# Performance work log

Hardware: AMD Instinct MI355X
Metric: run time of the kernel (lower is better)

Reference implementation:

```python
import jax, jax.numpy as jnp
import numpy as np

B, C, H, W = 4, 256, 128, 128
K = 3
BN = max(16, C // 4)  # 64
PAD = K // 2
EPS = 1e-5


def conv2d(x, w, b=None, pad=0):
    out = jax.lax.conv_general_dilated(
        x, w, (1, 1), [(pad, pad), (pad, pad)],
        dimension_numbers=("NCHW", "OIHW", "NCHW"))
    if b is not None:
        out = out + b[None, :, None, None]
    return out


def deform_conv2d(z, offset, mask, w, b):
    # torchvision modulated deform conv v2: offset [B,2*K*K,H,W] interleaved (dy,dx),
    # mask [B,K*K,H,W], kernel positions row-major, stride 1, pad PAD.
    Bz, Cb, Hz, Wz = z.shape
    K2 = K * K
    off = offset.reshape(Bz, K2, 2, Hz, Wz)
    ky, kx = jnp.meshgrid(jnp.arange(K), jnp.arange(K), indexing="ij")
    # sampling positions py/px: [B, K2, H, W]
    py = off[:, :, 0] + jnp.arange(Hz)[None, None, :, None] + (ky.reshape(K2) - PAD)[None, :, None, None]
    px = off[:, :, 1] + jnp.arange(Wz)[None, None, None, :] + (kx.reshape(K2) - PAD)[None, :, None, None]
    y0 = jnp.floor(py)
    x0 = jnp.floor(px)
    wy1 = py - y0  # frac weights
    wx1 = px - x0
    z_flat = z.reshape(Bz, Cb, Hz * Wz)

    def gather(yy, xx, wgt):
        valid = (yy >= 0) & (yy < Hz) & (xx >= 0) & (xx < Wz)
        yc = jnp.clip(yy, 0, Hz - 1).astype(jnp.int32)
        xc = jnp.clip(xx, 0, Wz - 1).astype(jnp.int32)
        idx = (yc * Wz + xc).reshape(Bz, K2 * Hz * Wz)
        g = jnp.take_along_axis(z_flat, idx[:, None, :], axis=2)  # [B, Cb, K2*H*W]
        g = g.reshape(Bz, Cb, K2, Hz, Wz)
        return g * (wgt * valid.astype(z.dtype))[:, None]

    val = (gather(y0, x0, (1 - wy1) * (1 - wx1))
           + gather(y0, x0 + 1, (1 - wy1) * wx1)
           + gather(y0 + 1, x0, wy1 * (1 - wx1))
           + gather(y0 + 1, x0 + 1, wy1 * wx1))
    val = val * mask[:, None]  # modulate: [B, Cb, K2, H, W]
    out = jnp.einsum("bckhw,ock->bohw", val, w.reshape(w.shape[0], Cb, K2))
    return out + b[None, :, None, None]


def setup_inputs() -> dict:
    key = jax.random.key(0)
    ks = jax.random.split(key, 11)
    s = 0.05
    return {
        "x": jax.random.normal(ks[0], (B, C, H, W), jnp.float32),
        "down_w": jax.random.normal(ks[1], (BN, C, 1, 1), jnp.float32) * s,
        "off_w": jax.random.normal(ks[2], (2 * K * K, BN, 3, 3), jnp.float32) * s,
        "off_b": jax.random.normal(ks[3], (2 * K * K,), jnp.float32) * s,
        "mask_w": jax.random.normal(ks[4], (K * K, BN, 3, 3), jnp.float32) * s,
        "mask_b": jax.random.normal(ks[5], (K * K,), jnp.float32) * s,
        "def_w": jax.random.normal(ks[6], (BN, BN, K, K), jnp.float32) * s,
        "def_b": jax.random.normal(ks[7], (BN,), jnp.float32) * s,
        "up_w": jax.random.normal(ks[8], (C, BN, 1, 1), jnp.float32) * s,
        "gamma": jnp.ones((C,), jnp.float32),
        "beta": jnp.zeros((C,), jnp.float32),
    }


def reference(x, down_w, off_w, off_b, mask_w, mask_b, def_w, def_b, up_w, gamma, beta):
    z = conv2d(x, down_w)                               # 1x1 down: [B, BN, H, W]
    offset = conv2d(z, off_w, off_b, pad=1)             # [B, 18, H, W]
    mask = jax.nn.sigmoid(conv2d(z, mask_w, mask_b, pad=1))  # [B, 9, H, W]
    z = deform_conv2d(z, offset, mask, def_w, def_b)    # [B, BN, H, W]
    z = conv2d(z, up_w)                                 # 1x1 up: [B, C, H, W]
    y = x + z
    # BatchNorm2d in training mode: batch statistics over (B, H, W), biased var
    mean = jnp.mean(y, axis=(0, 2, 3), keepdims=True)
    var = jnp.var(y, axis=(0, 2, 3), keepdims=True)
    yh = (y - mean) * jax.lax.rsqrt(var + EPS)
    yh = yh * gamma[None, :, None, None] + beta[None, :, None, None]
    return yh * jax.nn.sigmoid(yh)  # SiLU
```

## Files before the change

kernel.cpp:

```cpp
#include <hip/hip_runtime.h>
#include <hip/hip_bf16.h>


typedef __attribute__((ext_vector_type(8))) short bf16x8;
typedef __attribute__((ext_vector_type(4))) short bf16x4;
typedef __attribute__((ext_vector_type(4))) float f32x4;

#define HW   16384
#define CC   256
#define BNC  64

#define WS_STATS   0
#define WS_SS      131072
#define WS_FD      135168
#define WS_FOM     167936
#define WS_FDEF    204800
#define WS_FUP     278528
#define WS_ZBF     311296
#define WS_OM      8699904
#define WS_Z2      15777792

__device__ __forceinline__ short f2b(float f) {
    unsigned u = __float_as_uint(f);
    unsigned r = (u + 0x7FFFu + ((u >> 16) & 1u)) >> 16;
    return (short)r;
}
__device__ __forceinline__ float b2f(short s) {
    return __uint_as_float(((unsigned)(unsigned short)s) << 16);
}

__global__ void k_prep(const float* __restrict__ down_w, const float* __restrict__ off_w,
                       const float* __restrict__ mask_w, const float* __restrict__ def_w,
                       const float* __restrict__ up_w, char* __restrict__ ws) {
    int g = blockIdx.x * 256 + threadIdx.x;
    int row = g >> 6, lane = g & 63;
    if (row >= 172) return;
    int l15 = lane & 15, q = lane >> 4;
    short vals[8];
    short* dst;
    if (row < 32) {
        int nt = row >> 3, kk = row & 7;
        int n = nt * 16 + l15;
        for (int j = 0; j < 8; ++j) {
            int c = kk * 32 + q * 8 + j;
            vals[j] = f2b(down_w[n * 256 + c]);
        }
        dst = (short*)(ws + WS_FD) + row * 512 + lane * 8;
    } else if (row < 68) {
        int r = row - 32; int nt = r / 18, kk = r % 18;
        int n = nt * 16 + l15;
        for (int j = 0; j < 8; ++j) {
            int kap = kk * 32 + q * 8 + j; int k = kap >> 6, c = kap & 63;
            float v = 0.f;
            if (n < 18)      v = off_w[(n * 64 + c) * 9 + k];
            else if (n < 27) v = mask_w[((n - 18) * 64 + c) * 9 + k];
            vals[j] = f2b(v);
        }
        dst = (short*)(ws + WS_FOM) + r * 512 + lane * 8;
    } else if (row < 140) {
        int r = row - 68; int nt = r / 18, kk = r % 18;
        int n = nt * 16 + l15;
        int u = kk * 4 + q, k = u >> 3;
        for (int j = 0; j < 8; ++j) {
            int c = (u & 7) * 8 + j;
            vals[j] = f2b(def_w[(n * 64 + c) * 9 + k]);
        }
        dst = (short*)(ws + WS_FDEF) + r * 512 + lane * 8;
    } else {
        int r = row - 140; int nt = r >> 1, kk = r & 1;
        int o = nt * 16 + l15;
        for (int j = 0; j < 8; ++j) {
            int c = kk * 32 + q * 8 + j;
            vals[j] = f2b(up_w[o * 64 + c]);
        }
        dst = (short*)(ws + WS_FUP) + r * 512 + lane * 8;
    }
    for (int j = 0; j < 8; ++j) dst[j] = vals[j];
}

__global__ __launch_bounds__(256) void k_down(const float* __restrict__ x,
                                              const short* __restrict__ wfd,
                                              short* __restrict__ zbf) {
    __shared__ __align__(16) short xl[64 * 264];
    int blk = blockIdx.x;
    int b = blk >> 8;
    int hw0 = (blk & 255) * 64;
    int t = threadIdx.x;
    const float* xb = x + (size_t)b * CC * HW + hw0;
    int px = t & 63, w = t >> 6;
    for (int h = 0; h < 8; ++h) {
        int c0 = h * 32 + w * 8;
        bf16x8 pk;
        #pragma unroll
        for (int j = 0; j < 8; ++j)
            pk[j] = f2b(xb[(size_t)(c0 + j) * HW + px]);
        *(bf16x8*)(&xl[px * 264 + c0]) = pk;
    }
    __syncthreads();
    int lane = t & 63, wv = t >> 6;
    int l15 = lane & 15, q = lane >> 4;
    bf16x8 A[8];
    const short* xrow = &xl[(wv * 16 + l15) * 264];
    for (int kk = 0; kk < 8; ++kk)
        A[kk] = *(const bf16x8*)(xrow + kk * 32 + q * 8);
    const bf16x8* Bp = (const bf16x8*)wfd;
    size_t obase = ((size_t)b * HW + hw0 + wv * 16) * 64;
    for (int nt = 0; nt < 4; ++nt) {
        f32x4 acc = {0.f, 0.f, 0.f, 0.f};
        for (int kk = 0; kk < 8; ++kk) {
            bf16x8 Bf = Bp[(nt * 8 + kk) * 64 + lane];
            acc = __builtin_amdgcn_mfma_f32_16x16x32_bf16(A[kk], Bf, acc, 0, 0, 0);
        }
        int n = nt * 16 + l15;
        for (int r = 0; r < 4; ++r) {
            int prow = q * 4 + r;
            zbf[obase + (size_t)prow * 64 + n] = f2b(acc[r]);
        }
    }
}

__global__ __launch_bounds__(256) void k_offmask(const short* __restrict__ zbf,
                                                 const short* __restrict__ wfom,
                                                 const float* __restrict__ off_b,
                                                 const float* __restrict__ mask_b,
                                                 float* __restrict__ om) {
    int blk = blockIdx.x;
    int b = blk >> 8;
    int hw0 = (blk & 255) * 64;
    int y = hw0 >> 7, x0 = hw0 & 127;
    int t = threadIdx.x, lane = t & 63, wv = t >> 6;
    int l15 = lane & 15, q = lane >> 4;
    int xx0 = x0 + wv * 16 + l15;
    const short* zb = zbf + (size_t)b * HW * 64;
    f32x4 acc0 = {0, 0, 0, 0}, acc1 = {0, 0, 0, 0};
    const bf16x8* Bp = (const bf16x8*)wfom;
    for (int kk = 0; kk < 18; ++kk) {
        int k = kk >> 1;
        int yy = y + (k / 3) - 1;
        int xx = xx0 + (k % 3) - 1;
        int c0 = (kk & 1) * 32 + q * 8;
        bf16x8 A = {0, 0, 0, 0, 0, 0, 0, 0};
        if (yy >= 0 && yy < 128 && xx >= 0 && xx < 128)
            A = *(const bf16x8*)(zb + ((size_t)(yy * 128 + xx)) * 64 + c0);
        bf16x8 B0 = Bp[kk * 64 + lane];
        bf16x8 B1 = Bp[(18 + kk) * 64 + lane];
        acc0 = __builtin_amdgcn_mfma_f32_16x16x32_bf16(A, B0, acc0, 0, 0, 0);
        acc1 = __builtin_amdgcn_mfma_f32_16x16x32_bf16(A, B1, acc1, 0, 0, 0);
    }
    float* omb = om + ((size_t)b * HW + hw0 + wv * 16) * 27;
    for (int half = 0; half < 2; ++half) {
        f32x4 acc = half ? acc1 : acc0;
        int n = half * 16 + l15;
        if (n < 27) {
            for (int r = 0; r < 4; ++r) {
                int prow = q * 4 + r;
                float v = acc[r];
                if (n < 18) v += off_b[n];
                else { v += mask_b[n - 18]; v = 1.f / (1.f + __expf(-v)); }
                omb[prow * 27 + n] = v;
            }
        }
    }
}

__global__ __launch_bounds__(256) void k_deform(const short* __restrict__ zbf,
                                                const float* __restrict__ om,
                                                const short* __restrict__ wfdef,
                                                const float* __restrict__ def_b,
                                                short* __restrict__ z2) {
    __shared__ __align__(16) short ldsZ[169 * 64];
    __shared__ int4   pAi4[144];
    __shared__ float4 pAw4[144];
    __shared__ int    pAf[144];
    __shared__ __align__(16) short valA[18 * 64 * 8];
    int blk = blockIdx.x;
    int b = blk >> 10;
    int tile = blk & 1023;
    int yt = (tile >> 5) << 2, xt = (tile & 31) << 2;
    int sy0 = yt - 4; sy0 = sy0 < 0 ? 0 : (sy0 > 115 ? 115 : sy0);
    int sx0 = xt - 4; sx0 = sx0 < 0 ? 0 : (sx0 > 115 ? 115 : sx0);
    int t = threadIdx.x;
    const short* zbs = zbf + (size_t)b * HW * 64;
    for (int u = t; u < 1352; u += 256) {
        int r = u / 104, rem = u - r * 104;
        int p = rem >> 3, cg = rem & 7;
        int gp = (sy0 + r) * 128 + sx0 + p;
        int lpix = r * 13 + p;
        int slot = (cg + lpix) & 7;
        *(int4*)(&ldsZ[lpix * 64 + slot * 8]) = *(const int4*)(zbs + (size_t)gp * 64 + cg * 8);
    }
    if (t < 144) {
        int px = t / 9, k = t % 9;
        int oy = yt + (px >> 2), ox = xt + (px & 3);
        const float* p = om + ((size_t)b * HW + oy * 128 + ox) * 27;
        float dy = p[2 * k], dx = p[2 * k + 1], m = p[18 + k];
        float py  = (float)oy + (float)(k / 3 - 1) + dy;
        float pxf = (float)ox + (float)(k % 3 - 1) + dx;
        float fy = floorf(py), fx = floorf(pxf);
        int iy = (int)fy, ix = (int)fx;
        float wy = py - fy, wx = pxf - fx;
        float ww[4] = { (1.f - wy) * (1.f - wx) * m, (1.f - wy) * wx * m,
                        wy * (1.f - wx) * m,          wy * wx * m };
        bool flg = (iy >= sy0) && (iy + 1 <= sy0 + 12) && (ix >= sx0) && (ix + 1 <= sx0 + 12);
        int ys[2] = {iy, iy + 1}, xs[2] = {ix, ix + 1};
        int   ri[4]; float rw[4];
        for (int ci = 0; ci < 4; ++ci) {
            int cy = ys[ci >> 1], cx = xs[ci & 1];
            if (flg) {
                int lp = (cy - sy0) * 13 + (cx - sx0);
                ri[ci] = (lp << 6) | (lp & 7);
                rw[ci] = ww[ci];
            } else {
                bool v = (cy >= 0 && cy < 128 && cx >= 0 && cx < 128);
                ri[ci] = v ? (cy * 128 + cx) * 64 : 0;
                rw[ci] = v ? ww[ci] : 0.f;
            }
        }
        pAi4[t] = make_int4(ri[0], ri[1], ri[2], ri[3]);
        pAw4[t] = make_float4(rw[0], rw[1], rw[2], rw[3]);
        pAf[t]  = flg ? 1 : 0;
    }
    __syncthreads();
    for (int it = 0; it < 5; ++it) {
        int s = t + it * 256;
        if (s < 1152) {
            int px = s & 15, u = s >> 4;
            int k = u >> 3, cg = u & 7;
            int task = px * 9 + k;
            int4   idx = pAi4[task];
            float4 wt  = pAw4[task];
            int    flg = pAf[task];
            int   ii[4] = { idx.x, idx.y, idx.z, idx.w };
            float wwt[4] = { wt.x, wt.y, wt.z, wt.w };
            int cgs = cg * 8;
            float acc[8] = {0.f, 0.f, 0.f, 0.f, 0.f, 0.f, 0.f, 0.f};
            #pragma unroll
            for (int ci = 0; ci < 4; ++ci) {
                float w = wwt[ci];
                int4 d;
                if (flg) {
                    int v = ii[ci];
                    d = *(const int4*)(&ldsZ[(v & ~63) + (((cg + (v & 7)) & 7) << 3)]);
                } else {
                    d = *(const int4*)(zbs + ii[ci] + cgs);
                }
                int dp[4] = { d.x, d.y, d.z, d.w };
                #pragma unroll
                for (int p = 0; p < 4; ++p) {
                    float lo = __uint_as_float((unsigned)dp[p] << 16);
                    float hi = __uint_as_float((unsigned)dp[p] & 0xffff0000u);
                    acc[2 * p]     += w * lo;
                    acc[2 * p + 1] += w * hi;
                }
            }
            bf16x8 out;
            #pragma unroll
            for (int j = 0; j < 8; ++j) out[j] = f2b(acc[j]);
            *(bf16x8*)(&valA[s * 8]) = out;
        }
    }
    __syncthreads();
    int lane = t & 63, wv = t >> 6;
    int l15 = lane & 15, q = lane >> 4;
    f32x4 acc = {0, 0, 0, 0};
    const bf16x8* Bp = (const bf16x8*)wfdef;
    const bf16x8* Ap = (const bf16x8*)valA;
    for (int kk = 0; kk < 18; ++kk) {
        bf16x8 A  = Ap[kk * 64 + lane];
        bf16x8 Bf = Bp[(wv * 18 + kk) * 64 + lane];
        acc = __builtin_amdgcn_mfma_f32_16x16x32_bf16(A, Bf, acc, 0, 0, 0);
    }
    int n = wv * 16 + l15;
    float bias = def_b[n];
    short* z2b = z2 + (size_t)b * HW * 64;
    for (int r = 0; r < 4; ++r) {
        int prow = q * 4 + r;
        int hw = (yt + (prow >> 2)) * 128 + xt + (prow & 3);
        z2b[(size_t)hw * 64 + n] = f2b(acc[r] + bias);
    }
}

__global__ __launch_bounds__(256) void k_up(const short* __restrict__ z2,
                                            const short* __restrict__ wfup,
                                            const float* __restrict__ x,
                                            float* __restrict__ yout,
                                            float* __restrict__ stats) {
    __shared__ __align__(16) short yl[256 * 70];
    int blk = blockIdx.x;
    int b = blk >> 8;
    int hw0 = (blk & 255) * 64;
    int t = threadIdx.x, lane = t & 63, wv = t >> 6;
    int l15 = lane & 15, q = lane >> 4;
    const short* z2b = z2 + ((size_t)b * HW + hw0 + wv * 16) * 64;
    bf16x8 A0 = *(const bf16x8*)(z2b + (size_t)l15 * 64 + q * 8);
    bf16x8 A1 = *(const bf16x8*)(z2b + (size_t)l15 * 64 + 32 + q * 8);
    const bf16x8* Bp = (const bf16x8*)wfup;
    for (int nt = 0; nt < 16; ++nt) {
        f32x4 acc = {0, 0, 0, 0};
        acc = __builtin_amdgcn_mfma_f32_16x16x32_bf16(A0, Bp[(nt * 2 + 0) * 64 + lane], acc, 0, 0, 0);
        acc = __builtin_amdgcn_mfma_f32_16x16x32_bf16(A1, Bp[(nt * 2 + 1) * 64 + lane], acc, 0, 0, 0);
        int o = nt * 16 + l15;
        bf16x4 pk;
        #pragma unroll
        for (int r = 0; r < 4; ++r) pk[r] = f2b(acc[r]);
        *(bf16x4*)(&yl[o * 70 + wv * 16 + q * 4]) = pk;
    }
    __syncthreads();
    int i16 = t & 15, og = t >> 4;
    int bucket = blk & 63;
    size_t base = (size_t)b * CC * HW + hw0 + (size_t)i16 * 4;
    #pragma unroll
    for (int i = 0; i < 16; ++i) {
        int o = og + 16 * i;
        size_t pb = base + (size_t)o * HW;
        float4 xv = *(const float4*)(x + pb);
        bf16x4 uv = *(const bf16x4*)(&yl[o * 70 + i16 * 4]);
        float v0 = b2f(uv[0]) + xv.x;
        float v1 = b2f(uv[1]) + xv.y;
        float v2 = b2f(uv[2]) + xv.z;
        float v3 = b2f(uv[3]) + xv.w;
        *(float4*)(yout + pb) = make_float4(v0, v1, v2, v3);
        float s  = v0 + v1 + v2 + v3;
        float s2 = v0 * v0 + v1 * v1 + v2 * v2 + v3 * v3;
        #pragma unroll
        for (int m = 8; m >= 1; m >>= 1) { s += __shfl_xor(s, m); s2 += __shfl_xor(s2, m); }
        if (i16 == 0) {
            atomicAdd(&stats[bucket * 512 + o], s);
            atomicAdd(&stats[bucket * 512 + 256 + o], s2);
        }
    }
}

__global__ void k_stats(const float* __restrict__ stats, const float* __restrict__ gamma,
                        const float* __restrict__ beta, float* __restrict__ ss) {
    int o = threadIdx.x;
    float s = 0.f, s2 = 0.f;
    for (int u = 0; u < 64; ++u) { s += stats[u * 512 + o]; s2 += stats[u * 512 + 256 + o]; }
    float mean = s * (1.f / 65536.f);
    float var  = s2 * (1.f / 65536.f) - mean * mean;
    float rs = rsqrtf(var + 1e-5f);
    float sc = gamma[o] * rs;
    ss[o]       = sc;
    ss[256 + o] = beta[o] - mean * sc;
}

__global__ __launch_bounds__(256) void k_bn(float* __restrict__ y, const float* __restrict__ ss) {
    int g = blockIdx.x * 256 + threadIdx.x;
    int o = (g >> 10) & 255;
    float sc = ss[o], sh = ss[256 + o];
    float4* p = (float4*)y + (size_t)g * 4;
    for (int i = 0; i < 4; ++i) {
        float4 v = p[i];
        float vf[4] = { v.x, v.y, v.z, v.w };
        for (int j = 0; j < 4; ++j) {
            float h = vf[j] * sc + sh;
            vf[j] = h / (1.f + __expf(-h));
        }
        p[i] = make_float4(vf[0], vf[1], vf[2], vf[3]);
    }
}

extern "C" void kernel_launch(void* const* d_in, const int* in_sizes, int n_in,
                              void* d_out, int out_size, void* d_ws, size_t ws_size,
                              hipStream_t stream) {
    const float* x      = (const float*)d_in[0];
    const float* down_w = (const float*)d_in[1];
    const float* off_w  = (const float*)d_in[2];
    const float* off_b  = (const float*)d_in[3];
    const float* mask_w = (const float*)d_in[4];
    const float* mask_b = (const float*)d_in[5];
    const float* def_w  = (const float*)d_in[6];
    const float* def_b  = (const float*)d_in[7];
    const float* up_w   = (const float*)d_in[8];
    const float* gamma  = (const float*)d_in[9];
    const float* beta   = (const float*)d_in[10];
    char* ws = (char*)d_ws;
    float* stats = (float*)(ws + WS_STATS);
    float* ss    = (float*)(ws + WS_SS);
    short* wfd   = (short*)(ws + WS_FD);
    short* wfom  = (short*)(ws + WS_FOM);
    short* wfdef = (short*)(ws + WS_FDEF);
    short* wfup  = (short*)(ws + WS_FUP);
    short* zbf   = (short*)(ws + WS_ZBF);
    float* om    = (float*)(ws + WS_OM);
    short* z2    = (short*)(ws + WS_Z2);
    float* y     = (float*)d_out;

    hipMemsetAsync(stats, 0, 64 * 512 * sizeof(float), stream);
    hipLaunchKernelGGL(k_prep,    dim3(43),   dim3(256), 0, stream, down_w, off_w, mask_w, def_w, up_w, ws);
    hipLaunchKernelGGL(k_down,    dim3(1024), dim3(256), 0, stream, x, wfd, zbf);
    hipLaunchKernelGGL(k_offmask, dim3(1024), dim3(256), 0, stream, zbf, wfom, off_b, mask_b, om);
    hipLaunchKernelGGL(k_deform,  dim3(4096), dim3(256), 0, stream, zbf, om, wfdef, def_b, z2);
    hipLaunchKernelGGL(k_up,      dim3(1024), dim3(256), 0, stream, z2, wfup, x, y, stats);
    hipLaunchKernelGGL(k_stats,   dim3(1),    dim3(256), 0, stream, stats, gamma, beta, ss);
    hipLaunchKernelGGL(k_bn,      dim3(4096), dim3(256), 0, stream, y, ss);
}
```

Measured before the change: 246.5 us.

## Fuse BN stats and SiLU apply into up-projection kernel via grid barrier

The up-projection kernel now keeps its residual-sum outputs in registers, then uses an atomic-counter grid-wide barrier: the last block computes the BatchNorm scale/shift and every block spins until it is published, then applies BN and SiLU and writes the output once. This removes the separate stats and BN kernels along with the write-then-reread round trip of the 64 MB output tensor. In exchange it relies on all 1024 blocks being co-resident (launch bounds of 4 blocks per CU), which is required to avoid deadlock, and it raises register pressure by holding 16 float4 values per thread.

```diff
diff --git a/kernel.cpp b/kernel.cpp
--- a/kernel.cpp
+++ b/kernel.cpp
@@ -11,7 +11,8 @@
 #define BNC  64
 
 #define WS_STATS   0
-#define WS_SS      131072
+#define WS_CNT     131072
+#define WS_SSG     131136
 #define WS_FD      135168
 #define WS_FOM     167936
 #define WS_FDEF    204800
@@ -280,12 +281,18 @@
     }
 }
 
-__global__ __launch_bounds__(256) void k_up(const short* __restrict__ z2,
-                                            const short* __restrict__ wfup,
-                                            const float* __restrict__ x,
-                                            float* __restrict__ yout,
-                                            float* __restrict__ stats) {
+__global__ __launch_bounds__(256, 4) void k_up(const short* __restrict__ z2,
+                                               const short* __restrict__ wfup,
+                                               const float* __restrict__ x,
+                                               const float* __restrict__ gamma,
+                                               const float* __restrict__ beta,
+                                               float* __restrict__ yout,
+                                               float* __restrict__ stats,
+                                               unsigned* __restrict__ cnt,
+                                               float* __restrict__ ssG) {
     __shared__ __align__(16) short yl[256 * 70];
+    __shared__ float ssl[512];
+    __shared__ int lflag;
     int blk = blockIdx.x;
     int b = blk >> 8;
     int hw0 = (blk & 255) * 64;
@@ -309,6 +316,7 @@
     int i16 = t & 15, og = t >> 4;
     int bucket = blk & 63;
     size_t base = (size_t)b * CC * HW + hw0 + (size_t)i16 * 4;
+    float4 v[16];
     #pragma unroll
     for (int i = 0; i < 16; ++i) {
         int o = og + 16 * i;
@@ -319,7 +327,7 @@
         float v1 = b2f(uv[1]) + xv.y;
         float v2 = b2f(uv[2]) + xv.z;
         float v3 = b2f(uv[3]) + xv.w;
-        *(float4*)(yout + pb) = make_float4(v0, v1, v2, v3);
+        v[i] = make_float4(v0, v1, v2, v3);
         float s  = v0 + v1 + v2 + v3;
         float s2 = v0 * v0 + v1 * v1 + v2 * v2 + v3 * v3;
         #pragma unroll
@@ -329,34 +337,50 @@
             atomicAdd(&stats[bucket * 512 + 256 + o], s2);
         }
     }
-}
-
-__global__ void k_stats(const float* __restrict__ stats, const float* __restrict__ gamma,
-                        const float* __restrict__ beta, float* __restrict__ ss) {
-    int o = threadIdx.x;
-    float s = 0.f, s2 = 0.f;
-    for (int u = 0; u < 64; ++u) { s += stats[u * 512 + o]; s2 += stats[u * 512 + 256 + o]; }
-    float mean = s * (1.f / 65536.f);
-    float var  = s2 * (1.f / 65536.f) - mean * mean;
-    float rs = rsqrtf(var + 1e-5f);
-    float sc = gamma[o] * rs;
-    ss[o]       = sc;
-    ss[256 + o] = beta[o] - mean * sc;
-}
-
-__global__ __launch_bounds__(256) void k_bn(float* __restrict__ y, const float* __restrict__ ss) {
-    int g = blockIdx.x * 256 + threadIdx.x;
-    int o = (g >> 10) & 255;
-    float sc = ss[o], sh = ss[256 + o];
-    float4* p = (float4*)y + (size_t)g * 4;
-    for (int i = 0; i < 4; ++i) {
-        float4 v = p[i];
-        float vf[4] = { v.x, v.y, v.z, v.w };
-        for (int j = 0; j < 4; ++j) {
-            float h = vf[j] * sc + sh;
-            vf[j] = h / (1.f + __expf(-h));
-        }
-        p[i] = make_float4(vf[0], vf[1], vf[2], vf[3]);
+    __threadfence();
+    __syncthreads();
+    if (t == 0) {
+        unsigned old = __hip_atomic_fetch_add(cnt, 1u, __ATOMIC_ACQ_REL, __HIP_MEMORY_SCOPE_AGENT);
+        lflag = (old == 1023u) ? 1 : 0;
+    }
+    __syncthreads();
+    if (lflag) {
+        float s = 0.f, s2 = 0.f;
+        for (int u = 0; u < 64; ++u) {
+            s  += __hip_atomic_load(&stats[u * 512 + t],       __ATOMIC_RELAXED, __HIP_MEMORY_SCOPE_AGENT);
+            s2 += __hip_atomic_load(&stats[u * 512 + 256 + t], __ATOMIC_RELAXED, __HIP_MEMORY_SCOPE_AGENT);
+        }
+        float mean = s * (1.f / 65536.f);
+        float var  = s2 * (1.f / 65536.f) - mean * mean;
+        float rs = rsqrtf(var + 1e-5f);
+        float sc = gamma[t] * rs;
+        __hip_atomic_store(&ssG[t],       sc,                 __ATOMIC_RELAXED, __HIP_MEMORY_SCOPE_AGENT);
+        __hip_atomic_store(&ssG[256 + t], beta[t] - mean * sc, __ATOMIC_RELAXED, __HIP_MEMORY_SCOPE_AGENT);
+        __threadfence();
+        __syncthreads();
+        if (t == 0)
+            __hip_atomic_fetch_add(cnt, 1u, __ATOMIC_ACQ_REL, __HIP_MEMORY_SCOPE_AGENT);
+    }
+    if (t == 0) {
+        while (__hip_atomic_load(cnt, __ATOMIC_ACQUIRE, __HIP_MEMORY_SCOPE_AGENT) < 1025u)
+            __builtin_amdgcn_s_sleep(2);
+    }
+    __syncthreads();
+    ssl[t]       = __hip_atomic_load(&ssG[t],       __ATOMIC_RELAXED, __HIP_MEMORY_SCOPE_AGENT);
+    ssl[256 + t] = __hip_atomic_load(&ssG[256 + t], __ATOMIC_RELAXED, __HIP_MEMORY_SCOPE_AGENT);
+    __syncthreads();
+    #pragma unroll
+    for (int i = 0; i < 16; ++i) {
+        int o = og + 16 * i;
+        float sc = ssl[o], sh = ssl[256 + o];
+        size_t pb = base + (size_t)o * HW;
+        float4 vv = v[i];
+        float h0 = vv.x * sc + sh, h1 = vv.y * sc + sh;
+        float h2 = vv.z * sc + sh, h3 = vv.w * sc + sh;
+        *(float4*)(yout + pb) = make_float4(h0 / (1.f + __expf(-h0)),
+                                            h1 / (1.f + __expf(-h1)),
+                                            h2 / (1.f + __expf(-h2)),
+                                            h3 / (1.f + __expf(-h3)));
     }
 }
 
@@ -375,8 +399,9 @@
     const float* gamma  = (const float*)d_in[9];
     const float* beta   = (const float*)d_in[10];
     char* ws = (char*)d_ws;
-    float* stats = (float*)(ws + WS_STATS);
-    float* ss    = (float*)(ws + WS_SS);
+    float*    stats = (float*)(ws + WS_STATS);
+    unsigned* cnt   = (unsigned*)(ws + WS_CNT);
+    float*    ssG   = (float*)(ws + WS_SSG);
     short* wfd   = (short*)(ws + WS_FD);
     short* wfom  = (short*)(ws + WS_FOM);
     short* wfdef = (short*)(ws + WS_FDEF);
@@ -386,12 +411,10 @@
     short* z2    = (short*)(ws + WS_Z2);
     float* y     = (float*)d_out;
 
-    hipMemsetAsync(stats, 0, 64 * 512 * sizeof(float), stream);
+    hipMemsetAsync(ws, 0, WS_FD, stream);
     hipLaunchKernelGGL(k_prep,    dim3(43),   dim3(256), 0, stream, down_w, off_w, mask_w, def_w, up_w, ws);
     hipLaunchKernelGGL(k_down,    dim3(1024), dim3(256), 0, stream, x, wfd, zbf);
     hipLaunchKernelGGL(k_offmask, dim3(1024), dim3(256), 0, stream, zbf, wfom, off_b, mask_b, om);
     hipLaunchKernelGGL(k_deform,  dim3(4096), dim3(256), 0, stream, zbf, om, wfdef, def_b, z2);
-    hipLaunchKernelGGL(k_up,      dim3(1024), dim3(256), 0, stream, z2, wfup, x, y, stats);
-    hipLaunchKernelGGL(k_stats,   dim3(1),    dim3(256), 0, stream, stats, gamma, beta, ss);
-    hipLaunchKernelGGL(k_bn,      dim3(4096), dim3(256), 0, stream, y, ss);
-}
+    hipLaunchKernelGGL(k_up,      dim3(1024), dim3(256), 0, stream, z2, wfup, x, gamma, beta, y, stats, cnt, ssG);
+}
```

Result: slower. 464.5 us (+88.4%).
